# Optimization experiments

Hardware: AMD Instinct MI355X
Metric: run time of the kernel (lower is better)

The kernel has to match this reference:

```python
import jax, jax.numpy as jnp
import numpy as np

B, T, DIN, DOUT, RANK = 4, 1, 4096, 11008, 512


def setup_inputs() -> dict:
    key = jax.random.key(0)
    ks = jax.random.split(key, 7)
    inp = jax.random.normal(ks[0], (B, T, DIN), jnp.float32)
    weight = jax.random.normal(ks[1], (DOUT, DIN), jnp.float32) * (1.0 / np.sqrt(DIN))
    bias = jax.random.normal(ks[2], (DOUT,), jnp.float32) * 0.02
    U = jax.random.normal(ks[3], (DOUT, RANK), jnp.float32) * (1.0 / np.sqrt(RANK))
    S = jax.random.uniform(ks[4], (RANK,), jnp.float32, 0.1, 1.0)
    V = jax.random.normal(ks[5], (DIN, RANK), jnp.float32) * (1.0 / np.sqrt(DIN))
    scale = jax.random.uniform(ks[6], (DIN,), jnp.float32, 0.5, 1.5)
    threshold = jnp.full((1,), 0.674, jnp.float32)
    return {"input": inp, "weight": weight, "bias": bias, "U": U, "S": S,
            "V": V, "scale": scale, "threshold": threshold}


def reference(input, weight, bias, U, S, V, scale, threshold):
    # r_sparse mode, decoding path (num_tokens == 1)
    th = threshold[0]
    # mask from scaled magnitudes; piecewise-constant w.r.t. inputs
    s_mask = jax.lax.stop_gradient(
        (jnp.abs(input * scale[None, None, :]) > th).astype(input.dtype))
    # sparse GEMM on masked input: [B,T,DIN] x [DOUT,DIN]^T + bias
    sparse_out = jnp.einsum('btd,od->bto', input * s_mask, weight) + bias
    # low-rank compensation on the complement: x @ (V diag(S)) @ U^T
    lr = jnp.einsum('btd,dr->btr', input * (1.0 - s_mask), V * S[None, :])
    lr = jnp.einsum('btr,or->bto', lr, U)
    return sparse_out + lr
```

## Files before the change

kernel.cpp:

```cpp
#include <hip/hip_runtime.h>
#include <cmath>

constexpr int DIN  = 4096;
constexpr int DOUT = 11008;
constexpr int RANK = 512;
constexpr int NB   = 4;

constexpr int NCHUNK = 256;
constexpr int DCH    = DIN / NCHUNK;

constexpr int SPLITK = 2;
constexpr int ROWS   = 8;
constexpr int CHUNK  = 256;
constexpr int CH4    = CHUNK / 4;
constexpr int NCH    = DIN / SPLITK / CHUNK;
constexpr int NBUF   = 3;

#define GLOAD_LDS16(gsrc, ldst)                                                   \
    __builtin_amdgcn_global_load_lds(                                             \
        (const __attribute__((address_space(1))) void*)(gsrc),                    \
        (__attribute__((address_space(3))) void*)(ldst), 16, 0, 0)

#define WAITV(n) asm volatile("s_waitcnt vmcnt(" #n ")" ::: "memory")

__global__ __launch_bounds__(512)
void lr_partial_kernel(const float* __restrict__ x,
                       const float* __restrict__ scale,
                       const float* __restrict__ thp,
                       const float* __restrict__ V,
                       float* __restrict__ partial,
                       float* __restrict__ xs)
{
    __shared__ float xc[NB * DCH];
    const int chunk = blockIdx.x;
    const int t = threadIdx.x;
    const float th = thp[0];
    if (t < NB * DCH) {
        const int b = t / DCH, dd = t % DCH;
        const int d = chunk * DCH + dd;
        const float xv = x[b * DIN + d];
        const bool keep = fabsf(xv * scale[d]) > th;
        xc[t] = keep ? 0.f : xv;
        xs[b * DIN + d] = keep ? xv : 0.f;
    }
    __syncthreads();
    const int r = t;
    float a0 = 0.f, a1 = 0.f, a2 = 0.f, a3 = 0.f;
    #pragma unroll
    for (int dd = 0; dd < DCH; ++dd) {
        const float v = V[(size_t)(chunk * DCH + dd) * RANK + r];
        a0 = fmaf(xc[0 * DCH + dd], v, a0);
        a1 = fmaf(xc[1 * DCH + dd], v, a1);
        a2 = fmaf(xc[2 * DCH + dd], v, a2);
        a3 = fmaf(xc[3 * DCH + dd], v, a3);
    }
    float* p = partial + (size_t)chunk * (NB * RANK) + r;
    p[0 * RANK] = a0;
    p[1 * RANK] = a1;
    p[2 * RANK] = a2;
    p[3 * RANK] = a3;
}

__global__ __launch_bounds__(256)
void lr_reduce_kernel(const float* __restrict__ partial,
                      const float* __restrict__ S,
                      float* __restrict__ lr)
{
    const int t = blockIdx.x * 256 + threadIdx.x;
    const int idx = t >> 4;
    const int s = t & 15;
    float sum = 0.f;
    #pragma unroll
    for (int j = 0; j < 16; ++j)
        sum += partial[(size_t)(s * 16 + j) * (NB * RANK) + idx];
    #pragma unroll
    for (int m = 8; m >= 1; m >>= 1)
        sum += __shfl_xor(sum, m, 64);
    if (s == 0)
        lr[idx] = sum * S[idx & (RANK - 1)];
}

__global__ __launch_bounds__(256)
void rsparse_main_kernel(const float* __restrict__ xs,
                         const float* __restrict__ W,
                         const float* __restrict__ U,
                         const float* __restrict__ lr,
                         float* __restrict__ part)
{
    __shared__ float sbuf[NBUF * ROWS * CHUNK];
    const int tid  = threadIdx.x;
    const int wave = tid >> 6, lane = tid & 63;
    const int kh   = blockIdx.y;
    const int o0   = blockIdx.x * ROWS;
    const int kofs = kh * (DIN / SPLITK);
    const int r0   = wave * 2, r1 = r0 + 1;

    const float4* __restrict__ XS = (const float4*)xs;
    const int xbase4 = kofs / 4;

    const float* Wr0 = W + (size_t)(o0 + r0) * DIN + kofs + lane * 4;
    const float* Wr1 = W + (size_t)(o0 + r1) * DIN + kofs + lane * 4;

    auto STAGE = [&](int buf, int c) {
        GLOAD_LDS16(Wr0 + c * CHUNK, &sbuf[buf * (ROWS * CHUNK) + r0 * CHUNK]);
        GLOAD_LDS16(Wr1 + c * CHUNK, &sbuf[buf * (ROWS * CHUNK) + r1 * CHUNK]);
    };

    float acc0[NB] = {0.f, 0.f, 0.f, 0.f};
    float acc1[NB] = {0.f, 0.f, 0.f, 0.f};

    STAGE(0, 0);
    STAGE(1, 1);

    #pragma unroll
    for (int c = 0; c < NCH; ++c) {
        if (c + 2 < NCH)
            STAGE((c + 2) % NBUF, c + 2);

        const int ahead = (NCH - 1 - c) < 2 ? (NCH - 1 - c) : 2;
        if (ahead == 2)      WAITV(4);
        else if (ahead == 1) WAITV(2);
        else                 WAITV(0);
        __builtin_amdgcn_sched_barrier(0);

        const float4* wb = (const float4*)&sbuf[(c % NBUF) * (ROWS * CHUNK)];
        const float4 w0 = wb[r0 * CH4 + lane];
        const float4 w1 = wb[r1 * CH4 + lane];
        const int x4 = xbase4 + c * CH4 + lane;
        #pragma unroll
        for (int b = 0; b < NB; ++b) {
            const float4 xv = XS[b * 1024 + x4];
            acc0[b] = fmaf(w0.x, xv.x, acc0[b]);
            acc0[b] = fmaf(w0.y, xv.y, acc0[b]);
            acc0[b] = fmaf(w0.z, xv.z, acc0[b]);
            acc0[b] = fmaf(w0.w, xv.w, acc0[b]);
            acc1[b] = fmaf(w1.x, xv.x, acc1[b]);
            acc1[b] = fmaf(w1.y, xv.y, acc1[b]);
            acc1[b] = fmaf(w1.z, xv.z, acc1[b]);
            acc1[b] = fmaf(w1.w, xv.w, acc1[b]);
        }
    }

    if (kh == 0) {
        const float4* __restrict__ U0 = (const float4*)(U + (size_t)(o0 + r0) * RANK);
        const float4* __restrict__ U1 = (const float4*)(U + (size_t)(o0 + r1) * RANK);
        const float4* __restrict__ LR = (const float4*)lr;
        #pragma unroll
        for (int j = 0; j < 2; ++j) {
            const int c = (j << 6) + lane;
            const float4 u0 = U0[c];
            const float4 u1 = U1[c];
            #pragma unroll
            for (int b = 0; b < NB; ++b) {
                const float4 lv = LR[b * 128 + c];
                acc0[b] = fmaf(u0.x, lv.x, acc0[b]);
                acc0[b] = fmaf(u0.y, lv.y, acc0[b]);
                acc0[b] = fmaf(u0.z, lv.z, acc0[b]);
                acc0[b] = fmaf(u0.w, lv.w, acc0[b]);
                acc1[b] = fmaf(u1.x, lv.x, acc1[b]);
                acc1[b] = fmaf(u1.y, lv.y, acc1[b]);
                acc1[b] = fmaf(u1.z, lv.z, acc1[b]);
                acc1[b] = fmaf(u1.w, lv.w, acc1[b]);
            }
        }
    }

    #pragma unroll
    for (int b = 0; b < NB; ++b) {
        #pragma unroll
        for (int m = 32; m >= 1; m >>= 1) {
            acc0[b] += __shfl_xor(acc0[b], m, 64);
            acc1[b] += __shfl_xor(acc1[b], m, 64);
        }
    }

    if (lane == 0) {
        float* p = part + (size_t)kh * (NB * DOUT);
        #pragma unroll
        for (int b = 0; b < NB; ++b) {
            p[b * DOUT + o0 + r0] = acc0[b];
            p[b * DOUT + o0 + r1] = acc1[b];
        }
    }
}

__global__ __launch_bounds__(256)
void final_add_kernel(const float* __restrict__ part,
                      const float* __restrict__ bias,
                      float* __restrict__ out)
{
    const int i4 = blockIdx.x * 256 + threadIdx.x;
    const int o4 = i4 % (DOUT / 4);
    const float4 p0 = ((const float4*)part)[i4];
    const float4 p1 = ((const float4*)part)[NB * DOUT / 4 + i4];
    const float4 bv = ((const float4*)bias)[o4];
    float4 r;
    r.x = p0.x + p1.x + bv.x;
    r.y = p0.y + p1.y + bv.y;
    r.z = p0.z + p1.z + bv.z;
    r.w = p0.w + p1.w + bv.w;
    ((float4*)out)[i4] = r;
}

extern "C" void kernel_launch(void* const* d_in, const int* in_sizes, int n_in,
                              void* d_out, int out_size, void* d_ws, size_t ws_size,
                              hipStream_t stream)
{
    const float* x     = (const float*)d_in[0];
    const float* W     = (const float*)d_in[1];
    const float* bias  = (const float*)d_in[2];
    const float* U     = (const float*)d_in[3];
    const float* S     = (const float*)d_in[4];
    const float* V     = (const float*)d_in[5];
    const float* scale = (const float*)d_in[6];
    const float* thp   = (const float*)d_in[7];
    float* out = (float*)d_out;

    float* partial = (float*)d_ws;
    float* lr      = partial + (size_t)NCHUNK * NB * RANK;
    float* xs      = lr + NB * RANK;
    float* part    = xs + NB * DIN;

    lr_partial_kernel<<<NCHUNK, 512, 0, stream>>>(x, scale, thp, V, partial, xs);
    lr_reduce_kernel<<<(NB * RANK * 16) / 256, 256, 0, stream>>>(partial, S, lr);

    dim3 grid(DOUT / ROWS, SPLITK);
    rsparse_main_kernel<<<grid, 256, 0, stream>>>(xs, W, U, lr, part);
    final_add_kernel<<<(NB * DOUT / 4) / 256, 256, 0, stream>>>(part, bias, out);
}
```

Before: 47.88 us.

## Drop split-K and fuse bias epilogue into main GEMV kernel

Removes the two-way split-K in the main kernel so each block covers the full DIN reduction and writes the output directly with bias added, eliminating the final_add kernel launch and the partial buffer round-trip. The pipeline depth grows to four LDS buffers with three chunks in flight to cover the longer per-block loop. The trade-off is half as many blocks (1376), which lowers parallelism and latency hiding on a memory-bound weight stream.

```diff
diff --git a/kernel.cpp b/kernel.cpp
--- a/kernel.cpp
+++ b/kernel.cpp
@@ -9,12 +9,11 @@
 constexpr int NCHUNK = 256;
 constexpr int DCH    = DIN / NCHUNK;
 
-constexpr int SPLITK = 2;
 constexpr int ROWS   = 8;
 constexpr int CHUNK  = 256;
 constexpr int CH4    = CHUNK / 4;
-constexpr int NCH    = DIN / SPLITK / CHUNK;
-constexpr int NBUF   = 3;
+constexpr int NCH    = DIN / CHUNK;
+constexpr int NBUF   = 4;
 
 #define GLOAD_LDS16(gsrc, ldst)                                                   \
     __builtin_amdgcn_global_load_lds(                                             \
@@ -85,21 +84,19 @@
                          const float* __restrict__ W,
                          const float* __restrict__ U,
                          const float* __restrict__ lr,
-                         float* __restrict__ part)
+                         const float* __restrict__ bias,
+                         float* __restrict__ out)
 {
     __shared__ float sbuf[NBUF * ROWS * CHUNK];
     const int tid  = threadIdx.x;
     const int wave = tid >> 6, lane = tid & 63;
-    const int kh   = blockIdx.y;
     const int o0   = blockIdx.x * ROWS;
-    const int kofs = kh * (DIN / SPLITK);
     const int r0   = wave * 2, r1 = r0 + 1;
 
     const float4* __restrict__ XS = (const float4*)xs;
-    const int xbase4 = kofs / 4;
-
-    const float* Wr0 = W + (size_t)(o0 + r0) * DIN + kofs + lane * 4;
-    const float* Wr1 = W + (size_t)(o0 + r1) * DIN + kofs + lane * 4;
+
+    const float* Wr0 = W + (size_t)(o0 + r0) * DIN + lane * 4;
+    const float* Wr1 = W + (size_t)(o0 + r1) * DIN + lane * 4;
 
     auto STAGE = [&](int buf, int c) {
         GLOAD_LDS16(Wr0 + c * CHUNK, &sbuf[buf * (ROWS * CHUNK) + r0 * CHUNK]);
@@ -111,22 +108,23 @@
 
     STAGE(0, 0);
     STAGE(1, 1);
+    STAGE(2, 2);
 
     #pragma unroll
     for (int c = 0; c < NCH; ++c) {
-        if (c + 2 < NCH)
-            STAGE((c + 2) % NBUF, c + 2);
-
-        const int ahead = (NCH - 1 - c) < 2 ? (NCH - 1 - c) : 2;
-        if (ahead == 2)      WAITV(4);
-        else if (ahead == 1) WAITV(2);
-        else                 WAITV(0);
+        if (c + 3 < NCH)
+            STAGE((c + 3) & (NBUF - 1), c + 3);
+
+        if (c < NCH - 3)       WAITV(6);
+        else if (c == NCH - 3) WAITV(4);
+        else if (c == NCH - 2) WAITV(2);
+        else                   WAITV(0);
         __builtin_amdgcn_sched_barrier(0);
 
-        const float4* wb = (const float4*)&sbuf[(c % NBUF) * (ROWS * CHUNK)];
+        const float4* wb = (const float4*)&sbuf[(c & (NBUF - 1)) * (ROWS * CHUNK)];
         const float4 w0 = wb[r0 * CH4 + lane];
         const float4 w1 = wb[r1 * CH4 + lane];
-        const int x4 = xbase4 + c * CH4 + lane;
+        const int x4 = c * CH4 + lane;
         #pragma unroll
         for (int b = 0; b < NB; ++b) {
             const float4 xv = XS[b * 1024 + x4];
@@ -141,7 +139,7 @@
         }
     }
 
-    if (kh == 0) {
+    {
         const float4* __restrict__ U0 = (const float4*)(U + (size_t)(o0 + r0) * RANK);
         const float4* __restrict__ U1 = (const float4*)(U + (size_t)(o0 + r1) * RANK);
         const float4* __restrict__ LR = (const float4*)lr;
@@ -175,31 +173,13 @@
     }
 
     if (lane == 0) {
-        float* p = part + (size_t)kh * (NB * DOUT);
+        const float bi0 = bias[o0 + r0], bi1 = bias[o0 + r1];
         #pragma unroll
         for (int b = 0; b < NB; ++b) {
-            p[b * DOUT + o0 + r0] = acc0[b];
-            p[b * DOUT + o0 + r1] = acc1[b];
-        }
-    }
-}
-
-__global__ __launch_bounds__(256)
-void final_add_kernel(const float* __restrict__ part,
-                      const float* __restrict__ bias,
-                      float* __restrict__ out)
-{
-    const int i4 = blockIdx.x * 256 + threadIdx.x;
-    const int o4 = i4 % (DOUT / 4);
-    const float4 p0 = ((const float4*)part)[i4];
-    const float4 p1 = ((const float4*)part)[NB * DOUT / 4 + i4];
-    const float4 bv = ((const float4*)bias)[o4];
-    float4 r;
-    r.x = p0.x + p1.x + bv.x;
-    r.y = p0.y + p1.y + bv.y;
-    r.z = p0.z + p1.z + bv.z;
-    r.w = p0.w + p1.w + bv.w;
-    ((float4*)out)[i4] = r;
+            out[b * DOUT + o0 + r0] = acc0[b] + bi0;
+            out[b * DOUT + o0 + r1] = acc1[b] + bi1;
+        }
+    }
 }
 
 extern "C" void kernel_launch(void* const* d_in, const int* in_sizes, int n_in,
@@ -219,12 +199,8 @@
     float* partial = (float*)d_ws;
     float* lr      = partial + (size_t)NCHUNK * NB * RANK;
     float* xs      = lr + NB * RANK;
-    float* part    = xs + NB * DIN;
 
     lr_partial_kernel<<<NCHUNK, 512, 0, stream>>>(x, scale, thp, V, partial, xs);
     lr_reduce_kernel<<<(NB * RANK * 16) / 256, 256, 0, stream>>>(partial, S, lr);
-
-    dim3 grid(DOUT / ROWS, SPLITK);
-    rsparse_main_kernel<<<grid, 256, 0, stream>>>(xs, W, U, lr, part);
-    final_add_kernel<<<(NB * DOUT / 4) / 256, 256, 0, stream>>>(part, bias, out);
-}
+    rsparse_main_kernel<<<DOUT / ROWS, 256, 0, stream>>>(xs, W, U, lr, bias, out);
+}
```

Result: no change. 46.97 us (-1.9%).
